# Optimization experiments

Hardware: AMD Instinct MI355X
Metric: run time of the kernel (lower is better)

## Reference

```python
import jax, jax.numpy as jnp
import numpy as np

EPS = 1e-5
MIN_NORM = 1e-10

def _norm(x):
    return jnp.sqrt(jnp.clip(jnp.sum(x * x, axis=-1, keepdims=True), MIN_NORM, None))

def _proj(x):
    # clip points to the open unit Poincare ball
    n = _norm(x)
    max_n = 1.0 - EPS
    return jnp.where(n > max_n, x * (max_n / n), x)

def _artanh(x):
    return jnp.arctanh(jnp.clip(x, -1.0 + EPS, 1.0 - EPS))

def mob_add(u, v):
    uv = jnp.sum(u * v, axis=-1, keepdims=True)
    u2 = jnp.sum(u * u, axis=-1, keepdims=True)
    v2 = jnp.sum(v * v, axis=-1, keepdims=True)
    num = (1.0 + 2.0 * uv + v2) * u + (1.0 - u2) * v
    den = 1.0 + 2.0 * uv + u2 * v2
    return _proj(num / jnp.maximum(den, MIN_NORM))

def mob_mat_mul(M, x):
    # M: [Din, Dout], x: [B, Din] on the ball. Ganea Mobius matvec.
    x = _proj(x)
    Mx = x @ M
    x_n = _norm(x)
    Mx_n = _norm(Mx)
    return _proj(jnp.tanh(Mx_n / x_n * _artanh(x_n)) * (Mx / Mx_n))

def log_map_zero(y):
    n = _norm(y)
    return _artanh(n) * y / n

def exp_map_zero(v):
    n = _norm(v)
    return _proj(jnp.tanh(n) * v / n)

def mob_pointwise_prod(x, u):
    # coordinate-wise scale of hyperbolic x by gate u, in the tangent space at 0
    return exp_map_zero(log_map_zero(x) * u)

def _transition(W, h, U, x, b):
    Wh = mob_mat_mul(W, h)
    Ux = mob_mat_mul(U, x)
    return mob_add(mob_add(Wh, Ux), b)

def setup_inputs() -> dict:
    B, I, H = 2048, 1024, 1024
    Din, Dh = 2 * I, 2 * H
    k = (1.0 / H) ** 0.5
    key = jax.random.key(0)
    ks = jax.random.split(key, 8)
    return {
        "hyp_x": jax.random.normal(ks[0], (B, Din), jnp.float32) * 0.01,
        "hidden": jax.random.normal(ks[1], (B, Dh), jnp.float32) * 0.01,
        "w_z": jax.random.uniform(ks[2], (Dh, Dh), jnp.float32, -k, k),
        "w_r": jax.random.uniform(ks[3], (Dh, Dh), jnp.float32, -k, k),
        "w_h": jax.random.uniform(ks[4], (Dh, Dh), jnp.float32, -k, k),
        "u_z": jax.random.uniform(ks[5], (Din, Dh), jnp.float32, -k, k),
        "u_r": jax.random.uniform(ks[6], (Din, Dh), jnp.float32, -k, k),
        "b_z": jnp.zeros((Dh,), jnp.float32),
        "b_r": jnp.zeros((Dh,), jnp.float32),
        "b_h": jnp.zeros((Dh,), jnp.float32),
    }

def reference(hyp_x, hidden, w_z, w_r, w_h, u_z, u_r, b_z, b_r, b_h):
    hyp_x = _proj(hyp_x)
    hidden = _proj(hidden)
    z = jax.nn.sigmoid(log_map_zero(_transition(w_z, hidden, u_z, hyp_x, b_z)))
    r = jax.nn.sigmoid(log_map_zero(_transition(w_r, hidden, u_r, hyp_x, b_r)))
    r_point_h = mob_pointwise_prod(hidden, r)
    # NOTE: original source uses u_r (not u_h) here; replicated faithfully.
    h_tilde = _transition(w_h, r_point_h, u_r, hyp_x, b_h)
    minus_h_oplus_htilde = mob_add(-hidden, h_tilde)
    new_h = mob_add(hidden, mob_pointwise_prod(minus_h_oplus_htilde, z))
    return new_h
```

## Files before the change

### kernel.cpp

```cpp
#include <hip/hip_runtime.h>
#include <hip/hip_bf16.h>
#include <math.h>

#define EPS 1e-5f
#define MAXN (1.0f - EPS)
#define MINN 1e-10f

constexpr int D = 2048;
constexpr int LPT = 8;

typedef unsigned short u16;
typedef __bf16 bf16x8 __attribute__((ext_vector_type(8)));
typedef float floatx4 __attribute__((ext_vector_type(4)));


__device__ __forceinline__ u16 f2bf(float f) {
    union { float f; unsigned u; } v; v.f = f;
    unsigned r = v.u + 0x7FFFu + ((v.u >> 16) & 1u);
    return (u16)(r >> 16);
}

__device__ __forceinline__ float artanh_(float x) {
    x = fminf(fmaxf(x, -1.0f + EPS), 1.0f - EPS);
    return 0.5f * logf((1.0f + x) / (1.0f - x));
}

__device__ __forceinline__ float sigmoid_(float x) {
    return 1.0f / (1.0f + expf(-x));
}

__device__ __forceinline__ void gl_lds16(const u16* g, u16* l) {
    __builtin_amdgcn_global_load_lds(
        (const __attribute__((address_space(1))) unsigned int*)g,
        (__attribute__((address_space(3))) unsigned int*)l, 16, 0, 0);
}

__device__ __forceinline__ float block_sum(float v, float* sbuf) {
    #pragma unroll
    for (int off = 32; off >= 1; off >>= 1) v += __shfl_xor(v, off, 64);
    int w = threadIdx.x >> 6;
    __syncthreads();
    if ((threadIdx.x & 63) == 0) sbuf[w] = v;
    __syncthreads();
    return sbuf[0] + sbuf[1] + sbuf[2] + sbuf[3];
}

__device__ __forceinline__ void mmm_finish(float sum2, float g, float* coef, float* onorm) {
    float mxn = sqrtf(fmaxf(sum2, MINN));
    float tt  = tanhf(mxn * g);
    float on  = fminf(tt, MAXN);
    *coef = on / mxn;
    *onorm = on;
}

__device__ __forceinline__ float mob_add_frag(float* u, const float* v,
                                              float u2, float v2, float* sbuf) {
    float duv = 0.f;
    #pragma unroll
    for (int i = 0; i < LPT; ++i) duv += u[i] * v[i];
    duv = block_sum(duv, sbuf);
    float cu  = 1.f + 2.f * duv + v2;
    float cv  = 1.f - u2;
    float den = fmaxf(1.f + 2.f * duv + u2 * v2, MINN);
    float s2 = 0.f;
    #pragma unroll
    for (int i = 0; i < LPT; ++i) {
        float nm = cu * u[i] + cv * v[i];
        u[i] = nm;
        s2 += nm * nm;
    }
    s2 = block_sum(s2, sbuf);
    float n  = sqrtf(fmaxf(s2 / (den * den), MINN));
    float sc = ((n > MAXN) ? MAXN / n : 1.f) / den;
    #pragma unroll
    for (int i = 0; i < LPT; ++i) u[i] *= sc;
    return fminf(n, MAXN);
}


struct TransBatch { const float* W[5]; u16* Wt[5]; };

__global__ __launch_bounds__(256) void wtrans(TransBatch tb) {
    const float* W = tb.W[blockIdx.z];
    u16* Wt = tb.Wt[blockIdx.z];
    __shared__ float tile[32][33];
    int n0 = blockIdx.x * 32, k0 = blockIdx.y * 32;
    int tc = threadIdx.x & 31, tr = threadIdx.x >> 5;
    #pragma unroll
    for (int i = 0; i < 4; ++i) {
        int r = tr + i * 8;
        tile[r][tc] = W[(size_t)(k0 + r) * D + n0 + tc];
    }
    __syncthreads();
    #pragma unroll
    for (int i = 0; i < 4; ++i) {
        int r = tr + i * 8;
        Wt[(size_t)(n0 + r) * D + k0 + tc] = f2bf(tile[tc][r]);
    }
}


__global__ __launch_bounds__(256) void prep(
    const float* __restrict__ hx, const float* __restrict__ h,
    u16* __restrict__ hx_bf, u16* __restrict__ h_bf,
    float* __restrict__ h_proj, float* __restrict__ g_x, float* __restrict__ g_h) {
    __shared__ float sbuf[4];
    int b = blockIdx.x, t = threadIdx.x;
    size_t off = (size_t)b * D;

    {
        float xv[LPT]; float s = 0.f;
        #pragma unroll
        for (int i = 0; i < LPT; ++i) { xv[i] = hx[off + t + 256 * i]; s += xv[i] * xv[i]; }
        float n = sqrtf(fmaxf(block_sum(s, sbuf), MINN));
        float scale = (n > MAXN) ? MAXN / n : 1.0f;
        float xn = fminf(n, MAXN);
        #pragma unroll
        for (int i = 0; i < LPT; ++i) hx_bf[off + t + 256 * i] = f2bf(xv[i] * scale);
        if (t == 0) g_x[b] = artanh_(xn) / xn;
    }
    {
        float xv[LPT]; float s = 0.f;
        #pragma unroll
        for (int i = 0; i < LPT; ++i) { xv[i] = h[off + t + 256 * i]; s += xv[i] * xv[i]; }
        float n = sqrtf(fmaxf(block_sum(s, sbuf), MINN));
        float scale = (n > MAXN) ? MAXN / n : 1.0f;
        float xn = fminf(n, MAXN);
        #pragma unroll
        for (int i = 0; i < LPT; ++i) {
            float pv = xv[i] * scale;
            h_bf[off + t + 256 * i] = f2bf(pv);
            h_proj[off + t + 256 * i] = pv;
        }
        if (t == 0) g_h[b] = artanh_(xn) / xn;
    }
}


struct GemmBatch { const u16* A[4]; const u16* W[4]; float* C[4]; int koff[4]; int klen[4]; };

__global__ __launch_bounds__(256) void gemm_bt(GemmBatch gb) {
    int z = blockIdx.z;
    const u16* __restrict__ A = gb.A[z];
    const u16* __restrict__ W = gb.W[z];
    float* __restrict__ C = gb.C[z];
    int koff = gb.koff[z], klen = gb.klen[z];

    __shared__ u16 As[128 * 32];
    __shared__ u16 Ws[128 * 32];

    int t = threadIdx.x;
    int wave = t >> 6, lane = t & 63;
    int wr = wave >> 1, wc = wave & 1;
    int quad = lane >> 4, l16 = lane & 15;
    int brow = blockIdx.y * 128, bcol = blockIdx.x * 128;

    int ra = 32 * wave + (lane >> 2);
    int sa = (lane & 3) * 8;
    const u16* pa0 = A + (size_t)(brow + ra) * D + koff + sa;
    const u16* pa1 = pa0 + (size_t)16 * D;
    const u16* pw0 = W + (size_t)(bcol + ra) * D + koff + sa;
    const u16* pw1 = pw0 + (size_t)16 * D;
    u16* la0 = &As[(32 * wave) * 32];
    u16* la1 = &As[(32 * wave + 16) * 32];
    u16* lw0 = &Ws[(32 * wave) * 32];
    u16* lw1 = &Ws[(32 * wave + 16) * 32];

    floatx4 acc[4][4];
    #pragma unroll
    for (int i = 0; i < 4; ++i)
        #pragma unroll
        for (int j = 0; j < 4; ++j)
            #pragma unroll
            for (int e = 0; e < 4; ++e) acc[i][j][e] = 0.f;

    for (int k0 = 0; k0 < klen; k0 += 32) {
        __syncthreads();
        gl_lds16(pa0 + k0, la0);
        gl_lds16(pa1 + k0, la1);
        gl_lds16(pw0 + k0, lw0);
        gl_lds16(pw1 + k0, lw1);
        __syncthreads();

        bf16x8 af[4], bfv[4];
        #pragma unroll
        for (int i = 0; i < 4; ++i)
            af[i] = *(const bf16x8*)(&As[(wr * 64 + i * 16 + l16) * 32 + quad * 8]);
        #pragma unroll
        for (int j = 0; j < 4; ++j)
            bfv[j] = *(const bf16x8*)(&Ws[(wc * 64 + j * 16 + l16) * 32 + quad * 8]);
        #pragma unroll
        for (int i = 0; i < 4; ++i)
            #pragma unroll
            for (int j = 0; j < 4; ++j)
                acc[i][j] = __builtin_amdgcn_mfma_f32_16x16x32_bf16(af[i], bfv[j], acc[i][j], 0, 0, 0);
    }

    #pragma unroll
    for (int i = 0; i < 4; ++i) {
        #pragma unroll
        for (int j = 0; j < 4; ++j) {
            int row = brow + wr * 64 + i * 16 + quad * 4;
            int col = bcol + wc * 64 + j * 16 + l16;
            #pragma unroll
            for (int r = 0; r < 4; ++r)
                C[(size_t)(row + r) * D + col] = acc[i][j][r];
        }
    }
}


__global__ __launch_bounds__(256) void mid_kernel(
    const float* __restrict__ c_wz, const float* __restrict__ c_uz,
    const float* __restrict__ c_wr, const float* __restrict__ c_ur,
    const float* __restrict__ h_proj,
    const float* __restrict__ g_x, const float* __restrict__ g_h,
    const float* __restrict__ b_z, const float* __restrict__ b_r,
    float* __restrict__ z_out, float* __restrict__ uxr_out,
    u16* __restrict__ rph_bf, float* __restrict__ g_rph) {
    __shared__ float sbuf[4];
    int b = blockIdx.x, t = threadIdx.x;
    size_t off = (size_t)b * D;

    float wz[LPT], uz[LPT], wr2[LPT], ur2[LPT], hp[LPT], bz[LPT], br[LPT], zz[LPT];
    float swz = 0, suz = 0, swr = 0, sur = 0;
    #pragma unroll
    for (int i = 0; i < LPT; ++i) {
        int c = t + 256 * i;
        wz[i]  = c_wz[off + c];  swz += wz[i] * wz[i];
        uz[i]  = c_uz[off + c];  suz += uz[i] * uz[i];
        wr2[i] = c_wr[off + c];  swr += wr2[i] * wr2[i];
        ur2[i] = c_ur[off + c];  sur += ur2[i] * ur2[i];
        hp[i]  = h_proj[off + c];
        bz[i]  = b_z[c];
        br[i]  = b_r[c];
    }
    float gh = g_h[b], gx = g_x[b];
    swz = block_sum(swz, sbuf);
    suz = block_sum(suz, sbuf);
    swr = block_sum(swr, sbuf);
    sur = block_sum(sur, sbuf);

    float cwz, nwz, cuz, nuz, cwr, nwr, cur, nur;
    mmm_finish(swz, gh, &cwz, &nwz);
    mmm_finish(suz, gx, &cuz, &nuz);
    mmm_finish(swr, gh, &cwr, &nwr);
    mmm_finish(sur, gx, &cur, &nur);
    #pragma unroll
    for (int i = 0; i < LPT; ++i) {
        wz[i] *= cwz; uz[i] *= cuz; wr2[i] *= cwr; ur2[i] *= cur;
    }

    float sbz = 0, sbr2 = 0;
    #pragma unroll
    for (int i = 0; i < LPT; ++i) { sbz += bz[i] * bz[i]; sbr2 += br[i] * br[i]; }
    sbz  = block_sum(sbz, sbuf);
    sbr2 = block_sum(sbr2, sbuf);

    float n1 = mob_add_frag(wz, uz, nwz * nwz, nuz * nuz, sbuf);
    float n2 = mob_add_frag(wz, bz, n1 * n1, sbz, sbuf);
    float gz = artanh_(n2) / n2;
    #pragma unroll
    for (int i = 0; i < LPT; ++i) {
        zz[i] = sigmoid_(gz * wz[i]);
        z_out[off + t + 256 * i] = zz[i];
    }

    float n1r = mob_add_frag(wr2, ur2, nwr * nwr, nur * nur, sbuf);
    float n2r = mob_add_frag(wr2, br, n1r * n1r, sbr2, sbuf);
    float gr = artanh_(n2r) / n2r;
    #pragma unroll
    for (int i = 0; i < LPT; ++i) br[i] = sigmoid_(gr * wr2[i]);

    float sv = 0.f;
    #pragma unroll
    for (int i = 0; i < LPT; ++i) {
        float v = gh * hp[i] * br[i];
        wz[i] = v;
        sv += v * v;
    }
    sv = block_sum(sv, sbuf);
    float nv = sqrtf(fmaxf(sv, MINN));
    float th = fminf(tanhf(nv), MAXN);
    float cr = th / nv;
    #pragma unroll
    for (int i = 0; i < LPT; ++i) {
        rph_bf[off + t + 256 * i] = f2bf(wz[i] * cr);
        uxr_out[off + t + 256 * i] = ur2[i];
    }
    if (t == 0) g_rph[b] = artanh_(th) / th;
}


__global__ __launch_bounds__(256) void fin_kernel(
    const float* __restrict__ c_wh_a, const float* __restrict__ c_wh_b,
    const float* __restrict__ uxr,
    const float* __restrict__ z_in, const float* __restrict__ h_proj,
    const float* __restrict__ g_rph, const float* __restrict__ b_h,
    float* __restrict__ out) {
    __shared__ float sbuf[4];
    int b = blockIdx.x, t = threadIdx.x;
    size_t off = (size_t)b * D;

    float wh[LPT], ux[LPT], zz[LPT], hp[LPT], bh[LPT];
    float swh = 0, sux = 0, shp = 0, sbh = 0;
    #pragma unroll
    for (int i = 0; i < LPT; ++i) {
        int c = t + 256 * i;
        wh[i] = c_wh_a[off + c] + c_wh_b[off + c];
        swh += wh[i] * wh[i];
        ux[i] = uxr[off + c];   sux += ux[i] * ux[i];
        zz[i] = z_in[off + c];
        hp[i] = h_proj[off + c]; shp += hp[i] * hp[i];
        bh[i] = b_h[c];         sbh += bh[i] * bh[i];
    }
    swh = block_sum(swh, sbuf);
    sux = block_sum(sux, sbuf);
    shp = block_sum(shp, sbuf);
    sbh = block_sum(sbh, sbuf);

    float cwh, nwh;
    mmm_finish(swh, g_rph[b], &cwh, &nwh);
    #pragma unroll
    for (int i = 0; i < LPT; ++i) wh[i] *= cwh;

    float n1  = mob_add_frag(wh, ux, nwh * nwh, sux, sbuf);
    float nht = mob_add_frag(wh, bh, n1 * n1, sbh, sbuf);

    #pragma unroll
    for (int i = 0; i < LPT; ++i) ux[i] = -hp[i];
    float nm = mob_add_frag(ux, wh, shp, nht * nht, sbuf);

    float lm = artanh_(nm) / nm;
    float sv = 0.f;
    #pragma unroll
    for (int i = 0; i < LPT; ++i) {
        float v = lm * ux[i] * zz[i];
        ux[i] = v;
        sv += v * v;
    }
    sv = block_sum(sv, sbuf);
    float nv = sqrtf(fmaxf(sv, MINN));
    float th = fminf(tanhf(nv), MAXN);
    float ce = th / nv;
    #pragma unroll
    for (int i = 0; i < LPT; ++i) ux[i] *= ce;

    mob_add_frag(hp, ux, shp, th * th, sbuf);
    #pragma unroll
    for (int i = 0; i < LPT; ++i) out[off + t + 256 * i] = hp[i];
}


extern "C" void kernel_launch(void* const* d_in, const int* in_sizes, int n_in,
                              void* d_out, int out_size, void* d_ws, size_t ws_size,
                              hipStream_t stream) {
    const float* hyp_x  = (const float*)d_in[0];
    const float* hidden = (const float*)d_in[1];
    const float* w_z = (const float*)d_in[2];
    const float* w_r = (const float*)d_in[3];
    const float* w_h = (const float*)d_in[4];
    const float* u_z = (const float*)d_in[5];
    const float* u_r = (const float*)d_in[6];
    const float* b_z = (const float*)d_in[7];
    const float* b_r = (const float*)d_in[8];
    const float* b_h = (const float*)d_in[9];
    float* out = (float*)d_out;

    int B = in_sizes[1] / D;

    char* ws = (char*)d_ws;
    size_t o = 0;
    auto alloc = [&](size_t bytes) -> void* {
        void* p = ws + o;
        o += (bytes + 255) & ~(size_t)255;
        return p;
    };
    u16* wt[5];
    for (int i = 0; i < 5; ++i) wt[i] = (u16*)alloc((size_t)D * D * 2);
    u16* hx_bf   = (u16*)alloc((size_t)B * D * 2);
    u16* h_bf    = (u16*)alloc((size_t)B * D * 2);
    float* h_proj = (float*)alloc((size_t)B * D * 4);
    float* g_x   = (float*)alloc((size_t)B * 4);
    float* g_h   = (float*)alloc((size_t)B * 4);
    float* g_rph = (float*)alloc((size_t)B * 4);
    float* c0 = (float*)alloc((size_t)B * D * 4);
    float* c1 = (float*)alloc((size_t)B * D * 4);
    float* c2 = (float*)alloc((size_t)B * D * 4);
    float* c3 = (float*)alloc((size_t)B * D * 4);
    float* z_buf = (float*)alloc((size_t)B * D * 4);
    float* uxr   = (float*)alloc((size_t)B * D * 4);
    u16* rph     = (u16*)alloc((size_t)B * D * 2);

    TransBatch tb;
    tb.W[0] = w_z; tb.W[1] = w_r; tb.W[2] = w_h; tb.W[3] = u_z; tb.W[4] = u_r;
    for (int i = 0; i < 5; ++i) tb.Wt[i] = wt[i];
    wtrans<<<dim3(D / 32, D / 32, 5), 256, 0, stream>>>(tb);

    prep<<<dim3(B), 256, 0, stream>>>(hyp_x, hidden, hx_bf, h_bf, h_proj, g_x, g_h);

    GemmBatch g1;
    g1.A[0] = h_bf;  g1.W[0] = wt[0]; g1.C[0] = c0;
    g1.A[1] = hx_bf; g1.W[1] = wt[3]; g1.C[1] = c1;
    g1.A[2] = h_bf;  g1.W[2] = wt[1]; g1.C[2] = c2;
    g1.A[3] = hx_bf; g1.W[3] = wt[4]; g1.C[3] = c3;
    for (int i = 0; i < 4; ++i) { g1.koff[i] = 0; g1.klen[i] = D; }
    gemm_bt<<<dim3(D / 128, B / 128, 4), 256, 0, stream>>>(g1);

    mid_kernel<<<dim3(B), 256, 0, stream>>>(c0, c1, c2, c3, h_proj, g_x, g_h,
                                            b_z, b_r, z_buf, uxr, rph, g_rph);

    GemmBatch g2;
    g2.A[0] = rph; g2.W[0] = wt[2]; g2.C[0] = c2; g2.koff[0] = 0;    g2.klen[0] = D / 2;
    g2.A[1] = rph; g2.W[1] = wt[2]; g2.C[1] = c3; g2.koff[1] = D/2;  g2.klen[1] = D / 2;
    g2.A[2] = g2.A[0]; g2.W[2] = g2.W[0]; g2.C[2] = g2.C[0]; g2.koff[2] = 0; g2.klen[2] = 0;
    g2.A[3] = g2.A[0]; g2.W[3] = g2.W[0]; g2.C[3] = g2.C[0]; g2.koff[3] = 0; g2.klen[3] = 0;
    gemm_bt<<<dim3(D / 128, B / 128, 2), 256, 0, stream>>>(g2);

    fin_kernel<<<dim3(B), 256, 0, stream>>>(c2, c3, uxr, z_buf, h_proj, g_rph, b_h, out);
}
```

Measured before the change: 349.4 us.

## Deepen GEMM K-tile to 64 with swizzled LDS, 4-way split-K, vectorized transpose

The GEMM now stages a K-depth of 64 per iteration with an XOR-swizzled LDS layout, which halves the number of barrier round-trips and avoids LDS bank conflicts. The loop length becomes a template parameter so it can be fully specialized. The second GEMM is split four ways along K instead of two, giving more blocks; fin_kernel sums four partial buffers, which adds some extra memory traffic. The weight transpose uses 64x64 tiles with float4 loads and 16-byte packed bf16 stores.

```diff
diff --git a/kernel.cpp b/kernel.cpp
--- a/kernel.cpp
+++ b/kernel.cpp
@@ -83,19 +83,30 @@
 __global__ __launch_bounds__(256) void wtrans(TransBatch tb) {
     const float* W = tb.W[blockIdx.z];
     u16* Wt = tb.Wt[blockIdx.z];
-    __shared__ float tile[32][33];
-    int n0 = blockIdx.x * 32, k0 = blockIdx.y * 32;
-    int tc = threadIdx.x & 31, tr = threadIdx.x >> 5;
-    #pragma unroll
-    for (int i = 0; i < 4; ++i) {
-        int r = tr + i * 8;
-        tile[r][tc] = W[(size_t)(k0 + r) * D + n0 + tc];
+    __shared__ float tile[64 * 65];
+    int n0 = blockIdx.x * 64, k0 = blockIdx.y * 64;
+    int t = threadIdx.x;
+
+    int lr = t >> 4, lc = (t & 15) * 4;
+    #pragma unroll
+    for (int p = 0; p < 4; ++p) {
+        int r = lr + p * 16;
+        float4 v = *(const float4*)(W + (size_t)(k0 + r) * D + n0 + lc);
+        tile[r * 65 + lc + 0] = v.x;
+        tile[r * 65 + lc + 1] = v.y;
+        tile[r * 65 + lc + 2] = v.z;
+        tile[r * 65 + lc + 3] = v.w;
     }
     __syncthreads();
-    #pragma unroll
-    for (int i = 0; i < 4; ++i) {
-        int r = tr + i * 8;
-        Wt[(size_t)(n0 + r) * D + k0 + tc] = f2bf(tile[tc][r]);
+
+    int wn = t >> 3, ws = (t & 7) * 8;
+    #pragma unroll
+    for (int p = 0; p < 2; ++p) {
+        int n = wn + p * 32;
+        u16 pk[8];
+        #pragma unroll
+        for (int j = 0; j < 8; ++j) pk[j] = f2bf(tile[(ws + j) * 65 + n]);
+        *(uint4*)(Wt + (size_t)(n0 + n) * D + k0 + ws) = *(uint4*)pk;
     }
 }
 
@@ -137,17 +148,18 @@
 }
 
 
-struct GemmBatch { const u16* A[4]; const u16* W[4]; float* C[4]; int koff[4]; int klen[4]; };
-
+struct GemmBatch { const u16* A[4]; const u16* W[4]; float* C[4]; int koff[4]; };
+
+template<int KLEN>
 __global__ __launch_bounds__(256) void gemm_bt(GemmBatch gb) {
     int z = blockIdx.z;
     const u16* __restrict__ A = gb.A[z];
     const u16* __restrict__ W = gb.W[z];
     float* __restrict__ C = gb.C[z];
-    int koff = gb.koff[z], klen = gb.klen[z];
-
-    __shared__ u16 As[128 * 32];
-    __shared__ u16 Ws[128 * 32];
+    int koff = gb.koff[z];
+
+    __shared__ u16 As[128 * 64];
+    __shared__ u16 Ws[128 * 64];
 
     int t = threadIdx.x;
     int wave = t >> 6, lane = t & 63;
@@ -155,16 +167,12 @@
     int quad = lane >> 4, l16 = lane & 15;
     int brow = blockIdx.y * 128, bcol = blockIdx.x * 128;
 
-    int ra = 32 * wave + (lane >> 2);
-    int sa = (lane & 3) * 8;
-    const u16* pa0 = A + (size_t)(brow + ra) * D + koff + sa;
-    const u16* pa1 = pa0 + (size_t)16 * D;
-    const u16* pw0 = W + (size_t)(bcol + ra) * D + koff + sa;
-    const u16* pw1 = pw0 + (size_t)16 * D;
-    u16* la0 = &As[(32 * wave) * 32];
-    u16* la1 = &As[(32 * wave + 16) * 32];
-    u16* lw0 = &Ws[(32 * wave) * 32];
-    u16* lw1 = &Ws[(32 * wave + 16) * 32];
+    int srow = 32 * wave + (lane >> 3);
+    int sseg = (lane & 7) ^ ((lane >> 3) & 7);
+    const u16* pa = A + (size_t)(brow + srow) * D + koff + sseg * 8;
+    const u16* pw = W + (size_t)(bcol + srow) * D + koff + sseg * 8;
+    u16* lbA = &As[wave * 2048];
+    u16* lbW = &Ws[wave * 2048];
 
     floatx4 acc[4][4];
     #pragma unroll
@@ -174,26 +182,33 @@
             #pragma unroll
             for (int e = 0; e < 4; ++e) acc[i][j][e] = 0.f;
 
-    for (int k0 = 0; k0 < klen; k0 += 32) {
+    int xsw = l16 & 7;
+
+    for (int k0 = 0; k0 < KLEN; k0 += 64) {
         __syncthreads();
-        gl_lds16(pa0 + k0, la0);
-        gl_lds16(pa1 + k0, la1);
-        gl_lds16(pw0 + k0, lw0);
-        gl_lds16(pw1 + k0, lw1);
+        #pragma unroll
+        for (int i = 0; i < 4; ++i) {
+            gl_lds16(pa + (size_t)(8 * i) * D + k0, lbA + i * 512);
+            gl_lds16(pw + (size_t)(8 * i) * D + k0, lbW + i * 512);
+        }
         __syncthreads();
 
-        bf16x8 af[4], bfv[4];
-        #pragma unroll
-        for (int i = 0; i < 4; ++i)
-            af[i] = *(const bf16x8*)(&As[(wr * 64 + i * 16 + l16) * 32 + quad * 8]);
-        #pragma unroll
-        for (int j = 0; j < 4; ++j)
-            bfv[j] = *(const bf16x8*)(&Ws[(wc * 64 + j * 16 + l16) * 32 + quad * 8]);
-        #pragma unroll
-        for (int i = 0; i < 4; ++i)
+        #pragma unroll
+        for (int kk = 0; kk < 2; ++kk) {
+            bf16x8 af[4], bfv[4];
+            int ps = ((kk * 4 + quad) ^ xsw) * 8;
+            #pragma unroll
+            for (int i = 0; i < 4; ++i)
+                af[i] = *(const bf16x8*)(&As[(wr * 64 + i * 16 + l16) * 64 + ps]);
             #pragma unroll
             for (int j = 0; j < 4; ++j)
-                acc[i][j] = __builtin_amdgcn_mfma_f32_16x16x32_bf16(af[i], bfv[j], acc[i][j], 0, 0, 0);
+                bfv[j] = *(const bf16x8*)(&Ws[(wc * 64 + j * 16 + l16) * 64 + ps]);
+            #pragma unroll
+            for (int i = 0; i < 4; ++i)
+                #pragma unroll
+                for (int j = 0; j < 4; ++j)
+                    acc[i][j] = __builtin_amdgcn_mfma_f32_16x16x32_bf16(af[i], bfv[j], acc[i][j], 0, 0, 0);
+        }
     }
 
     #pragma unroll
@@ -293,7 +308,8 @@
 
 
 __global__ __launch_bounds__(256) void fin_kernel(
-    const float* __restrict__ c_wh_a, const float* __restrict__ c_wh_b,
+    const float* __restrict__ p0, const float* __restrict__ p1,
+    const float* __restrict__ p2, const float* __restrict__ p3,
     const float* __restrict__ uxr,
     const float* __restrict__ z_in, const float* __restrict__ h_proj,
     const float* __restrict__ g_rph, const float* __restrict__ b_h,
@@ -307,7 +323,7 @@
     #pragma unroll
     for (int i = 0; i < LPT; ++i) {
         int c = t + 256 * i;
-        wh[i] = c_wh_a[off + c] + c_wh_b[off + c];
+        wh[i] = p0[off + c] + p1[off + c] + p2[off + c] + p3[off + c];
         swh += wh[i] * wh[i];
         ux[i] = uxr[off + c];   sux += ux[i] * ux[i];
         zz[i] = z_in[off + c];
@@ -395,7 +411,7 @@
     TransBatch tb;
     tb.W[0] = w_z; tb.W[1] = w_r; tb.W[2] = w_h; tb.W[3] = u_z; tb.W[4] = u_r;
     for (int i = 0; i < 5; ++i) tb.Wt[i] = wt[i];
-    wtrans<<<dim3(D / 32, D / 32, 5), 256, 0, stream>>>(tb);
+    wtrans<<<dim3(D / 64, D / 64, 5), 256, 0, stream>>>(tb);
 
     prep<<<dim3(B), 256, 0, stream>>>(hyp_x, hidden, hx_bf, h_bf, h_proj, g_x, g_h);
 
@@ -404,18 +420,19 @@
     g1.A[1] = hx_bf; g1.W[1] = wt[3]; g1.C[1] = c1;
     g1.A[2] = h_bf;  g1.W[2] = wt[1]; g1.C[2] = c2;
     g1.A[3] = hx_bf; g1.W[3] = wt[4]; g1.C[3] = c3;
-    for (int i = 0; i < 4; ++i) { g1.koff[i] = 0; g1.klen[i] = D; }
-    gemm_bt<<<dim3(D / 128, B / 128, 4), 256, 0, stream>>>(g1);
+    for (int i = 0; i < 4; ++i) g1.koff[i] = 0;
+    gemm_bt<2048><<<dim3(D / 128, B / 128, 4), 256, 0, stream>>>(g1);
 
     mid_kernel<<<dim3(B), 256, 0, stream>>>(c0, c1, c2, c3, h_proj, g_x, g_h,
                                             b_z, b_r, z_buf, uxr, rph, g_rph);
 
     GemmBatch g2;
-    g2.A[0] = rph; g2.W[0] = wt[2]; g2.C[0] = c2; g2.koff[0] = 0;    g2.klen[0] = D / 2;
-    g2.A[1] = rph; g2.W[1] = wt[2]; g2.C[1] = c3; g2.koff[1] = D/2;  g2.klen[1] = D / 2;
-    g2.A[2] = g2.A[0]; g2.W[2] = g2.W[0]; g2.C[2] = g2.C[0]; g2.koff[2] = 0; g2.klen[2] = 0;
-    g2.A[3] = g2.A[0]; g2.W[3] = g2.W[0]; g2.C[3] = g2.C[0]; g2.koff[3] = 0; g2.klen[3] = 0;
-    gemm_bt<<<dim3(D / 128, B / 128, 2), 256, 0, stream>>>(g2);
-
-    fin_kernel<<<dim3(B), 256, 0, stream>>>(c2, c3, uxr, z_buf, h_proj, g_rph, b_h, out);
-}
+    float* cb[4] = {c0, c1, c2, c3};
+    for (int s = 0; s < 4; ++s) {
+        g2.A[s] = rph; g2.W[s] = wt[2]; g2.C[s] = cb[s]; g2.koff[s] = s * 512;
+    }
+    gemm_bt<512><<<dim3(D / 128, B / 128, 4), 256, 0, stream>>>(g2);
+
+    fin_kernel<<<dim3(B), 256, 0, stream>>>(c0, c1, c2, c3, uxr, z_buf, h_proj,
+                                            g_rph, b_h, out);
+}
```

Result: faster. 338.0 us (-3.3%).
